# Kernel optimization log

Measured on AMD Instinct MI355X. Metric: run time of the kernel, lower is better.

The kernel has to match this reference:

```python
import jax, jax.numpy as jnp
import numpy as np

D_MODEL = 1024
N_HEADS = 16
D_FF = 4096
EPS = 1e-6


def layernorm(x, alpha, bias):
    # torch.std uses Bessel correction (ddof=1)
    mean = jnp.mean(x, axis=-1, keepdims=True)
    std = jnp.std(x, axis=-1, keepdims=True, ddof=1)
    return alpha * (x - mean) / (std + EPS) + bias


def setup_inputs() -> dict:
    key = jax.random.key(0)
    ks = jax.random.split(key, 12)
    s = 1.0 / np.sqrt(D_MODEL)
    sf = 1.0 / np.sqrt(D_FF)
    return {
        "x": jax.random.normal(ks[0], (2, 2048, D_MODEL), jnp.float32),
        "mask": jnp.ones((2, 1, 1, 2048), jnp.int32),
        "wq": jax.random.normal(ks[1], (D_MODEL, D_MODEL), jnp.float32) * s,
        "wk": jax.random.normal(ks[2], (D_MODEL, D_MODEL), jnp.float32) * s,
        "wv": jax.random.normal(ks[3], (D_MODEL, D_MODEL), jnp.float32) * s,
        "wo": jax.random.normal(ks[4], (D_MODEL, D_MODEL), jnp.float32) * s,
        "wo_b": jnp.zeros((D_MODEL,), jnp.float32),
        "w1": jax.random.normal(ks[5], (D_MODEL, D_FF), jnp.float32) * s,
        "b1": jnp.zeros((D_FF,), jnp.float32),
        "w2": jax.random.normal(ks[6], (D_FF, D_MODEL), jnp.float32) * sf,
        "b2": jnp.zeros((D_MODEL,), jnp.float32),
        "alpha1": jnp.ones((D_MODEL,), jnp.float32),
        "bias1": jnp.zeros((D_MODEL,), jnp.float32),
        "alpha2": jnp.ones((D_MODEL,), jnp.float32),
        "bias2": jnp.zeros((D_MODEL,), jnp.float32),
    }


def reference(x, mask, wq, wk, wv, wo, wo_b, w1, b1, w2, b2,
              alpha1, bias1, alpha2, bias2):
    B, S, D = x.shape
    h, dk = N_HEADS, D_MODEL // N_HEADS
    # projections -> [B, h, S, dk]
    q = (x @ wq).reshape(B, S, h, dk).transpose(0, 2, 1, 3)
    k = (x @ wk).reshape(B, S, h, dk).transpose(0, 2, 1, 3)
    v = (x @ wv).reshape(B, S, h, dk).transpose(0, 2, 1, 3)
    scores = jnp.einsum('bhqd,bhkd->bhqk', q, k) / jnp.sqrt(jnp.float32(dk))
    scores = jnp.where(mask == 0, jnp.float32(-1e9), scores)
    attn = jax.nn.softmax(scores, axis=-1)
    ctx = jnp.einsum('bhqk,bhkd->bhqd', attn, v)
    ctx = ctx.transpose(0, 2, 1, 3).reshape(B, S, D)
    attn_out = ctx @ wo + wo_b
    x = layernorm(x + attn_out, alpha1, bias1)
    ff = jax.nn.relu(x @ w1 + b1) @ w2 + b2
    x = layernorm(x + ff, alpha2, bias2)
    return x
```

## Files before the change

### kernel.cpp

```cpp
#include <hip/hip_runtime.h>
#include <hip/hip_bf16.h>

#define D_MODEL 1024
#define N_HEADS 16
#define DK      64
#define SEQ     2048
#define BATCH   2
#define D_FF    4096
#define ROWS    (BATCH*SEQ)
#define LN_EPS  1e-6f
#define SSTR    72
#define KTILE   128
#define PSTR    136

typedef __hip_bfloat16 bf16;
typedef __attribute__((ext_vector_type(8))) short frag8;
typedef __attribute__((ext_vector_type(4))) float facc4;

__device__ inline float bf2f(unsigned short u){ return __uint_as_float(((unsigned)u) << 16); }
__device__ inline float toF(bf16 v){ return __bfloat162float(v); }
__device__ inline unsigned short f2bu(float f){ bf16 h = __float2bfloat16(f); return *reinterpret_cast<unsigned short*>(&h); }

__device__ inline float ld1(const void* p, size_t idx, bool f32) {
    return f32 ? ((const float*)p)[idx] : toF(((const bf16*)p)[idx]);
}

struct U8 { unsigned short v[8]; };
__device__ inline U8 ld8bf(const void* p, size_t idx, bool f32) {
    U8 r;
    if (!f32) {
        *reinterpret_cast<uint4*>(r.v) = *reinterpret_cast<const uint4*>((const unsigned short*)p + idx);
    } else {
        const float* f = (const float*)p + idx;
        const float4 a = *reinterpret_cast<const float4*>(f);
        const float4 b = *reinterpret_cast<const float4*>(f + 4);
        r.v[0]=f2bu(a.x); r.v[1]=f2bu(a.y); r.v[2]=f2bu(a.z); r.v[3]=f2bu(a.w);
        r.v[4]=f2bu(b.x); r.v[5]=f2bu(b.y); r.v[6]=f2bu(b.z); r.v[7]=f2bu(b.w);
    }
    return r;
}

__device__ inline void gld16(const void* g, void* l) {
    __builtin_amdgcn_global_load_lds(
        reinterpret_cast<const __attribute__((address_space(1))) void*>(
            reinterpret_cast<uintptr_t>(g)),
        reinterpret_cast<__attribute__((address_space(3))) void*>(
            (unsigned int)reinterpret_cast<uintptr_t>(l)),
        16, 0, 0);
}

__global__ void probe_kernel(const void* __restrict__ xp, int* __restrict__ flag) {
    __shared__ int hit;
    if (threadIdx.x == 0) hit = 0;
    __syncthreads();
    const bf16* p = (const bf16*)xp;
    int bad = 0;
    for (int i = threadIdx.x; i < 8192; i += 256) {
        float v = fabsf(toF(p[i]));
        if (!(v <= 1e5f)) bad = 1;
    }
    if (bad) atomicOr(&hit, 1);
    __syncthreads();
    if (threadIdx.x == 0) *flag = hit;
}

__global__ __launch_bounds__(256) void xcvt_kernel(const void* __restrict__ x,
    bf16* __restrict__ out, const int* __restrict__ flagp)
{
    const bool f32 = (*flagp) != 0;
    const size_t i = ((size_t)blockIdx.x * 256 + threadIdx.x) * 8;
    U8 d = ld8bf(x, i, f32);
    *reinterpret_cast<uint4*>(out + i) = *reinterpret_cast<const uint4*>(d.v);
}

__global__ __launch_bounds__(256) void transpose_kernel(const void* __restrict__ W,
    bf16* __restrict__ WT, int K, int N, const int* __restrict__ flagp)
{
    const bool f32 = (*flagp) != 0;
    __shared__ float tile[32][33];
    const int tx = threadIdx.x, ty = threadIdx.y;
    const int n0 = blockIdx.x * 32, k0 = blockIdx.y * 32;
    #pragma unroll
    for (int r = 0; r < 4; ++r)
        tile[ty + 8*r][tx] = ld1(W, (size_t)(k0 + ty + 8*r) * N + n0 + tx, f32);
    __syncthreads();
    #pragma unroll
    for (int r = 0; r < 4; ++r)
        WT[(size_t)(n0 + ty + 8*r) * K + k0 + tx] = __float2bfloat16(tile[tx][ty + 8*r]);
}

__global__ __launch_bounds__(256) void vtrans_kernel(const bf16* __restrict__ V,
    bf16* __restrict__ VT)
{
    __shared__ unsigned short tile[32][33];
    const int tx = threadIdx.x, ty = threadIdx.y;
    const int s0 = blockIdx.x * 32, d0 = blockIdx.y * 32;
    const int bh = blockIdx.z, b = bh >> 4, h = bh & 15;
    #pragma unroll
    for (int r = 0; r < 4; ++r)
        tile[ty + 8*r][tx] = *reinterpret_cast<const unsigned short*>(
            V + ((size_t)(b * SEQ + s0 + ty + 8*r)) * D_MODEL + h * DK + d0 + tx);
    __syncthreads();
    #pragma unroll
    for (int r = 0; r < 4; ++r)
        *reinterpret_cast<unsigned short*>(
            VT + ((size_t)(bh * DK + d0 + ty + 8*r)) * SEQ + s0 + tx) = tile[tx][ty + 8*r];
}

template<bool RELU, bool BIAS, int NMAT, int SPLITK>
__global__ __launch_bounds__(256) void mgemm_kernel(const bf16* __restrict__ A,
    const bf16* __restrict__ BT, const void* __restrict__ bias,
    bf16* __restrict__ C, int M, int N, int K, const int* __restrict__ flagp)
{
    const bool inF32 = (*flagp) != 0;

    __shared__ unsigned short sA[128 * 64];
    __shared__ unsigned short sB[128 * 64];

    int which = 0, colb = blockIdx.x;
    if (NMAT > 1) { which = blockIdx.x >> 3; colb = blockIdx.x & 7; }
    const int kslice = (SPLITK > 1) ? blockIdx.z : 0;
    const int Kspan  = K / SPLITK;
    const int kbase  = kslice * Kspan;
    const bf16* Bp = BT + (size_t)which * N * K;
    bf16*       Cp = C  + (size_t)which * M * N + (size_t)kslice * M * N;

    const int row0 = blockIdx.y * 128;
    const int col0 = colb * 128;

    const int t    = threadIdx.x;
    const int wave = t >> 6;
    const int lane = t & 63;
    const int lm   = lane & 15;
    const int q    = lane >> 4;
    const int wm   = (wave & 1) * 64;
    const int wn   = (wave >> 1) * 64;

    facc4 acc[4][4];
    #pragma unroll
    for (int i = 0; i < 4; ++i)
        #pragma unroll
        for (int j = 0; j < 4; ++j)
            acc[i][j] = (facc4){0.f, 0.f, 0.f, 0.f};

    for (int k0 = kbase; k0 < kbase + Kspan; k0 += 64) {
        __syncthreads();
        #pragma unroll
        for (int j = 0; j < 4; ++j) {
            const int ch = (wave * 4 + j) * 64 + lane;
            const int r  = ch >> 3;
            const int cs = ch & 7;
            const int c  = cs ^ (r & 7);
            gld16(A  + (size_t)(row0 + r) * K + k0 + 8 * c, &sA[(wave * 4 + j) * 512]);
            gld16(Bp + (size_t)(col0 + r) * K + k0 + 8 * c, &sB[(wave * 4 + j) * 512]);
        }
        __syncthreads();

        #pragma unroll
        for (int kk = 0; kk < 64; kk += 32) {
            const int cr = (kk >> 3) + q;
            frag8 af[4], bfr[4];
            #pragma unroll
            for (int im = 0; im < 4; ++im) {
                const int m = wm + 16 * im + lm;
                af[im] = *reinterpret_cast<const frag8*>(&sA[m * 64 + ((cr ^ (m & 7)) << 3)]);
            }
            #pragma unroll
            for (int in = 0; in < 4; ++in) {
                const int n = wn + 16 * in + lm;
                bfr[in] = *reinterpret_cast<const frag8*>(&sB[n * 64 + ((cr ^ (n & 7)) << 3)]);
            }
            #pragma unroll
            for (int im = 0; im < 4; ++im)
                #pragma unroll
                for (int in = 0; in < 4; ++in)
                    acc[im][in] = __builtin_amdgcn_mfma_f32_16x16x32_bf16(af[im], bfr[in], acc[im][in], 0, 0, 0);
        }
    }

    #pragma unroll
    for (int in = 0; in < 4; ++in) {
        const int col = col0 + wn + 16*in + lm;
        float bv = 0.f;
        if (BIAS && kslice == 0) bv = ld1(bias, col, inF32);
        #pragma unroll
        for (int im = 0; im < 4; ++im) {
            #pragma unroll
            for (int r = 0; r < 4; ++r) {
                const int row = row0 + wm + 16*im + 4*q + r;
                float v = acc[im][in][r] + bv;
                if (RELU) v = fmaxf(v, 0.f);
                Cp[(size_t)row * N + col] = __float2bfloat16(v);
            }
        }
    }
}

__global__ __launch_bounds__(256) void fattn_kernel(
    const bf16* __restrict__ Qg, const bf16* __restrict__ Kg,
    const bf16* __restrict__ VTg, const int* __restrict__ mask,
    bf16* __restrict__ ctx)
{
    __shared__ unsigned short sK[128 * 64];
    __shared__ unsigned short sV[64 * 128];
    __shared__ unsigned short PsU[4 * 16 * PSTR];
    __shared__ float madd[KTILE];

    const int t    = threadIdx.x;
    const int qt   = blockIdx.x;
    const int h    = blockIdx.y;
    const int b    = blockIdx.z;
    const int q0   = qt * 64;
    const int bh   = b * N_HEADS + h;
    const int wave = t >> 6;
    const int lane = t & 63;
    const int lm   = lane & 15;
    const int qd   = lane >> 4;

    unsigned short* Qs = PsU;
    {
        const int sr = t >> 2, sd0 = (t & 3) * 16;
        const unsigned short* src = (const unsigned short*)
            (Qg + ((size_t)(b * SEQ + q0 + sr)) * D_MODEL + h * DK + sd0);
        unsigned short qi[16], qo[16];
        *reinterpret_cast<uint4*>(&qi[0]) = *reinterpret_cast<const uint4*>(src);
        *reinterpret_cast<uint4*>(&qi[8]) = *reinterpret_cast<const uint4*>(src + 8);
        #pragma unroll
        for (int u = 0; u < 16; ++u) qo[u] = f2bu(bf2f(qi[u]) * 0.125f);
        *reinterpret_cast<uint4*>(&Qs[sr * SSTR + sd0])     = *reinterpret_cast<const uint4*>(&qo[0]);
        *reinterpret_cast<uint4*>(&Qs[sr * SSTR + sd0 + 8]) = *reinterpret_cast<const uint4*>(&qo[8]);
    }
    __syncthreads();
    frag8 qf[2];
    #pragma unroll
    for (int s2 = 0; s2 < 2; ++s2)
        qf[s2] = *reinterpret_cast<const frag8*>(&Qs[(16 * wave + lm) * SSTR + 32 * s2 + 8 * qd]);

    facc4 accO[4];
    float m_r[4], l_r[4];
    #pragma unroll
    for (int r = 0; r < 4; ++r) { m_r[r] = -1e30f; l_r[r] = 0.f; }
    #pragma unroll
    for (int in = 0; in < 4; ++in) accO[in] = (facc4){0.f, 0.f, 0.f, 0.f};

    for (int kt = 0; kt < SEQ / KTILE; ++kt) {
        const int k0 = kt * KTILE;
        __syncthreads();

        #pragma unroll
        for (int j = 0; j < 4; ++j) {
            const int ch = (wave * 4 + j) * 64 + lane;
            const int rK = ch >> 3, cK = (ch & 7) ^ (rK & 7);
            gld16(Kg + ((size_t)(b * SEQ + k0 + rK)) * D_MODEL + h * DK + 8 * cK,
                  &sK[(wave * 4 + j) * 512]);
            const int rV = ch >> 4, cV = (ch & 15) ^ (rV & 15);
            gld16(VTg + ((size_t)(bh * DK + rV)) * SEQ + k0 + 8 * cV,
                  &sV[(wave * 4 + j) * 512]);
        }
        if (t < KTILE) madd[t] = (mask[b * SEQ + k0 + t] == 0) ? -1e9f : 0.f;
        __syncthreads();

        facc4 accS[8];
        #pragma unroll
        for (int i = 0; i < 8; ++i) accS[i] = (facc4){0.f, 0.f, 0.f, 0.f};
        #pragma unroll
        for (int i = 0; i < 8; ++i) {
            #pragma unroll
            for (int s2 = 0; s2 < 2; ++s2) {
                const int cr = 4 * s2 + qd;
                frag8 kf = *reinterpret_cast<const frag8*>(
                    &sK[(16 * i + lm) * 64 + ((cr ^ (lm & 7)) << 3)]);
                accS[i] = __builtin_amdgcn_mfma_f32_16x16x32_bf16(qf[s2], kf, accS[i], 0, 0, 0);
            }
        }

        float madv[8];
        #pragma unroll
        for (int i = 0; i < 8; ++i) madv[i] = madd[16 * i + lm];

        float mx[4];
        #pragma unroll
        for (int r = 0; r < 4; ++r) {
            float m0 = -1e30f;
            #pragma unroll
            for (int i = 0; i < 8; ++i) m0 = fmaxf(m0, accS[i][r] + madv[i]);
            #pragma unroll
            for (int off = 1; off < 16; off <<= 1) m0 = fmaxf(m0, __shfl_xor(m0, off));
            mx[r] = m0;
        }

        float alpha[4], mn[4], psum[4];
        #pragma unroll
        for (int r = 0; r < 4; ++r) {
            mn[r] = fmaxf(m_r[r], mx[r]);
            alpha[r] = __expf(m_r[r] - mn[r]);
            m_r[r] = mn[r];
            psum[r] = 0.f;
        }
        unsigned short* Pw = &PsU[wave * 16 * PSTR];
        #pragma unroll
        for (int i = 0; i < 8; ++i) {
            #pragma unroll
            for (int r = 0; r < 4; ++r) {
                float p = __expf(accS[i][r] + madv[i] - mn[r]);
                psum[r] += p;
                Pw[(qd * 4 + r) * PSTR + 16 * i + lm] = f2bu(p);
            }
        }
        #pragma unroll
        for (int r = 0; r < 4; ++r) {
            float s = psum[r];
            #pragma unroll
            for (int off = 1; off < 16; off <<= 1) s += __shfl_xor(s, off);
            l_r[r] = l_r[r] * alpha[r] + s;
            #pragma unroll
            for (int in = 0; in < 4; ++in) accO[in][r] *= alpha[r];
        }

        #pragma unroll
        for (int c = 0; c < 4; ++c) {
            frag8 pf = *reinterpret_cast<const frag8*>(&Pw[lm * PSTR + 32 * c + 8 * qd]);
            #pragma unroll
            for (int in = 0; in < 4; ++in) {
                const int cr = 4 * c + qd;
                frag8 vf = *reinterpret_cast<const frag8*>(
                    &sV[(16 * in + lm) * 128 + ((cr ^ lm) << 3)]);
                accO[in] = __builtin_amdgcn_mfma_f32_16x16x32_bf16(pf, vf, accO[in], 0, 0, 0);
            }
        }
    }

    float inv[4];
    #pragma unroll
    for (int r = 0; r < 4; ++r) inv[r] = 1.f / l_r[r];
    #pragma unroll
    for (int in = 0; in < 4; ++in)
        #pragma unroll
        for (int r = 0; r < 4; ++r)
            ctx[((size_t)(b * SEQ + q0 + 16 * wave + qd * 4 + r)) * D_MODEL + h * DK + 16 * in + lm]
                = __float2bfloat16(accO[in][r] * inv[r]);
}

template<bool BASE_WS, bool OUT_WS>
__global__ __launch_bounds__(256) void ln_kernel(const void* __restrict__ base,
    const bf16* __restrict__ addv, const bf16* __restrict__ addv2,
    const void* __restrict__ alpha, const void* __restrict__ bias,
    void* __restrict__ outp, const int* __restrict__ flagp)
{
    const bool inF32 = (*flagp) != 0;
    __shared__ float vals[D_MODEL];
    __shared__ float red[256];
    const int row = blockIdx.x, tid = threadIdx.x;

    float lsum = 0.f;
    for (int i = tid; i < D_MODEL; i += 256) {
        const size_t off = (size_t)row * D_MODEL + i;
        float v = (BASE_WS ? toF(((const bf16*)base)[off]) : ld1(base, off, inF32)) + toF(addv[off]);
        if (addv2) v += toF(addv2[off]);
        vals[i] = v; lsum += v;
    }
    red[tid] = lsum; __syncthreads();
    for (int s = 128; s > 0; s >>= 1) { if (tid < s) red[tid] += red[tid + s]; __syncthreads(); }
    const float mean = red[0] / (float)D_MODEL; __syncthreads();

    float lsq = 0.f;
    for (int i = tid; i < D_MODEL; i += 256) { float dd = vals[i] - mean; lsq += dd * dd; }
    red[tid] = lsq; __syncthreads();
    for (int s = 128; s > 0; s >>= 1) { if (tid < s) red[tid] += red[tid + s]; __syncthreads(); }
    const float var = red[0] / (float)(D_MODEL - 1);
    const float inv = 1.f / (sqrtf(var) + LN_EPS);

    for (int i = tid; i < D_MODEL; i += 256) {
        const size_t off = (size_t)row * D_MODEL + i;
        const float y = ld1(alpha, i, inF32) * (vals[i] - mean) * inv + ld1(bias, i, inF32);
        if (OUT_WS || !inF32) ((bf16*)outp)[off] = __float2bfloat16(y);
        else                  ((float*)outp)[off] = y;
    }
}

extern "C" void kernel_launch(void* const* d_in, const int* in_sizes, int n_in,
                              void* d_out, int out_size, void* d_ws, size_t ws_size,
                              hipStream_t stream)
{
    const void* x    = d_in[0];
    const int*  mask = (const int*)d_in[1];
    const void* wq   = d_in[2];
    const void* wk   = d_in[3];
    const void* wv   = d_in[4];
    const void* wo   = d_in[5];
    const void* wo_b = d_in[6];
    const void* w1   = d_in[7];
    const void* b1   = d_in[8];
    const void* w2   = d_in[9];
    const void* b2   = d_in[10];
    const void* al1  = d_in[11];
    const void* bi1  = d_in[12];
    const void* al2  = d_in[13];
    const void* bi2  = d_in[14];

    const size_t MB = 1024 * 1024;
    char* ws = (char*)d_ws;
    const bool SPLIT = ws_size >= 64 * MB + 4096;
    if (!SPLIT && ws_size < 56 * MB + 4096) return;

    bf16* Qb    = (bf16*)(ws + 0 * MB);
    bf16* Kb    = (bf16*)(ws + 8 * MB);
    bf16* Vb    = (bf16*)(ws + 16 * MB);
    bf16* Xb    = (bf16*)(ws + 24 * MB);
    bf16* VTb   = (bf16*)(ws + 24 * MB);
    bf16* WQKVT = (bf16*)(ws + 32 * MB);
    bf16* CTXb  = (bf16*)(ws + 32 * MB);
    bf16* W2T   = (bf16*)(ws + 32 * MB);
    bf16* WOT   = (bf16*)(ws + 0 * MB);
    bf16* ATT0  = (bf16*)(ws + 48 * MB);
    bf16* ATT1  = (bf16*)(ws + 56 * MB);
    bf16* W1T   = (bf16*)(ws + 48 * MB);
    bf16* X20   = (bf16*)(ws + 48 * MB);
    bf16* X21   = (bf16*)(ws + 56 * MB);
    bf16* X1b   = (bf16*)(ws + 40 * MB);
    bf16* FFb   = (bf16*)(ws + 0 * MB);
    int*  flagp = (int*)(ws + (SPLIT ? 64 : 56) * MB);

    probe_kernel<<<1, 256, 0, stream>>>(x, flagp);
    xcvt_kernel<<<dim3(ROWS * D_MODEL / 2048), 256, 0, stream>>>(x, Xb, flagp);

    dim3 tb(32, 8);
    transpose_kernel<<<dim3(32, 32), tb, 0, stream>>>(wq, WQKVT,           D_MODEL, D_MODEL, flagp);
    transpose_kernel<<<dim3(32, 32), tb, 0, stream>>>(wk, WQKVT + 1048576, D_MODEL, D_MODEL, flagp);
    transpose_kernel<<<dim3(32, 32), tb, 0, stream>>>(wv, WQKVT + 2097152, D_MODEL, D_MODEL, flagp);

    mgemm_kernel<false, false, 3, 1><<<dim3(24, 32), 256, 0, stream>>>(
        Xb, WQKVT, nullptr, Qb, ROWS, D_MODEL, D_MODEL, flagp);

    vtrans_kernel<<<dim3(SEQ / 32, 2, BATCH * N_HEADS), tb, 0, stream>>>(Vb, VTb);

    fattn_kernel<<<dim3(SEQ / 64, N_HEADS, BATCH), 256, 0, stream>>>(Qb, Kb, VTb, mask, CTXb);

    transpose_kernel<<<dim3(32, 32), tb, 0, stream>>>(wo, WOT, D_MODEL, D_MODEL, flagp);

    if (SPLIT) {
        mgemm_kernel<false, true, 1, 2><<<dim3(8, 32, 2), 256, 0, stream>>>(
            CTXb, WOT, wo_b, ATT0, ROWS, D_MODEL, D_MODEL, flagp);
        ln_kernel<false, true><<<ROWS, 256, 0, stream>>>(x, ATT0, ATT1, al1, bi1, X1b, flagp);
    } else {
        mgemm_kernel<false, true, 1, 1><<<dim3(8, 32), 256, 0, stream>>>(
            CTXb, WOT, wo_b, ATT0, ROWS, D_MODEL, D_MODEL, flagp);
        ln_kernel<false, true><<<ROWS, 256, 0, stream>>>(x, ATT0, nullptr, al1, bi1, X1b, flagp);
    }

    transpose_kernel<<<dim3(128, 32), tb, 0, stream>>>(w1, W1T, D_MODEL, D_FF, flagp);
    mgemm_kernel<true, true, 1, 1><<<dim3(32, 32), 256, 0, stream>>>(
        X1b, W1T, b1, FFb, ROWS, D_FF, D_MODEL, flagp);

    transpose_kernel<<<dim3(32, 128), tb, 0, stream>>>(w2, W2T, D_FF, D_MODEL, flagp);

    if (SPLIT) {
        mgemm_kernel<false, true, 1, 2><<<dim3(8, 32, 2), 256, 0, stream>>>(
            FFb, W2T, b2, X20, ROWS, D_MODEL, D_FF, flagp);
        ln_kernel<true, false><<<ROWS, 256, 0, stream>>>(X1b, X20, X21, al2, bi2, d_out, flagp);
    } else {
        mgemm_kernel<false, true, 1, 1><<<dim3(8, 32), 256, 0, stream>>>(
            FFb, W2T, b2, X20, ROWS, D_MODEL, D_FF, flagp);
        ln_kernel<true, false><<<ROWS, 256, 0, stream>>>(X1b, X20, nullptr, al2, bi2, d_out, flagp);
    }
}
```

Baseline: 419.1 us.

## Double attention query tile to 128 rows and batch square weight transposes

The flash-attention kernel now handles 128 query rows per block with 8 waves (512 threads) instead of 64 rows with 4. Each K/V tile staged in shared memory is therefore reused by twice as many queries, halving global K/V traffic per query, at the cost of a larger P buffer and fewer, heavier blocks. In the large-workspace path, the wq/wk/wv/wo transposes are merged into one launch with all weight transposes issued up front, and buffers are re-laid out so no transposed weight is overwritten. The small-workspace path keeps the old launch sequence but also uses the new attention configuration.

```diff
diff --git a/kernel.cpp b/kernel.cpp
--- a/kernel.cpp
+++ b/kernel.cpp
@@ -89,6 +89,26 @@
         WT[(size_t)(n0 + ty + 8*r) * K + k0 + tx] = __float2bfloat16(tile[tx][ty + 8*r]);
 }
 
+__global__ __launch_bounds__(256) void transpose4_kernel(const void* __restrict__ w0,
+    const void* __restrict__ w1, const void* __restrict__ w2, const void* __restrict__ w3,
+    bf16* __restrict__ WT4, const int* __restrict__ flagp)
+{
+    const bool f32 = (*flagp) != 0;
+    const int which = blockIdx.z;
+    const void* W = (which == 0) ? w0 : (which == 1) ? w1 : (which == 2) ? w2 : w3;
+    bf16* WT = WT4 + (size_t)which * D_MODEL * D_MODEL;
+    __shared__ float tile[32][33];
+    const int tx = threadIdx.x, ty = threadIdx.y;
+    const int n0 = blockIdx.x * 32, k0 = blockIdx.y * 32;
+    #pragma unroll
+    for (int r = 0; r < 4; ++r)
+        tile[ty + 8*r][tx] = ld1(W, (size_t)(k0 + ty + 8*r) * D_MODEL + n0 + tx, f32);
+    __syncthreads();
+    #pragma unroll
+    for (int r = 0; r < 4; ++r)
+        WT[(size_t)(n0 + ty + 8*r) * D_MODEL + k0 + tx] = __float2bfloat16(tile[tx][ty + 8*r]);
+}
+
 __global__ __launch_bounds__(256) void vtrans_kernel(const bf16* __restrict__ V,
     bf16* __restrict__ VT)
 {
@@ -196,21 +216,21 @@
     }
 }
 
-__global__ __launch_bounds__(256) void fattn_kernel(
+__global__ __launch_bounds__(512) void fattn_kernel(
     const bf16* __restrict__ Qg, const bf16* __restrict__ Kg,
     const bf16* __restrict__ VTg, const int* __restrict__ mask,
     bf16* __restrict__ ctx)
 {
     __shared__ unsigned short sK[128 * 64];
     __shared__ unsigned short sV[64 * 128];
-    __shared__ unsigned short PsU[4 * 16 * PSTR];
+    __shared__ unsigned short PsU[8 * 16 * PSTR];
     __shared__ float madd[KTILE];
 
     const int t    = threadIdx.x;
     const int qt   = blockIdx.x;
     const int h    = blockIdx.y;
     const int b    = blockIdx.z;
-    const int q0   = qt * 64;
+    const int q0   = qt * 128;
     const int bh   = b * N_HEADS + h;
     const int wave = t >> 6;
     const int lane = t & 63;
@@ -248,14 +268,14 @@
         __syncthreads();
 
         #pragma unroll
-        for (int j = 0; j < 4; ++j) {
-            const int ch = (wave * 4 + j) * 64 + lane;
+        for (int j = 0; j < 2; ++j) {
+            const int ch = (wave * 2 + j) * 64 + lane;
             const int rK = ch >> 3, cK = (ch & 7) ^ (rK & 7);
             gld16(Kg + ((size_t)(b * SEQ + k0 + rK)) * D_MODEL + h * DK + 8 * cK,
-                  &sK[(wave * 4 + j) * 512]);
+                  &sK[(wave * 2 + j) * 512]);
             const int rV = ch >> 4, cV = (ch & 15) ^ (rV & 15);
             gld16(VTg + ((size_t)(bh * DK + rV)) * SEQ + k0 + 8 * cV,
-                  &sV[(wave * 4 + j) * 512]);
+                  &sV[(wave * 2 + j) * 512]);
         }
         if (t < KTILE) madd[t] = (mask[b * SEQ + k0 + t] == 0) ? -1e9f : 0.f;
         __syncthreads();
@@ -400,65 +420,95 @@
 
     const size_t MB = 1024 * 1024;
     char* ws = (char*)d_ws;
-    const bool SPLIT = ws_size >= 64 * MB + 4096;
-    if (!SPLIT && ws_size < 56 * MB + 4096) return;
-
-    bf16* Qb    = (bf16*)(ws + 0 * MB);
-    bf16* Kb    = (bf16*)(ws + 8 * MB);
-    bf16* Vb    = (bf16*)(ws + 16 * MB);
-    bf16* Xb    = (bf16*)(ws + 24 * MB);
-    bf16* VTb   = (bf16*)(ws + 24 * MB);
-    bf16* WQKVT = (bf16*)(ws + 32 * MB);
-    bf16* CTXb  = (bf16*)(ws + 32 * MB);
-    bf16* W2T   = (bf16*)(ws + 32 * MB);
-    bf16* WOT   = (bf16*)(ws + 0 * MB);
-    bf16* ATT0  = (bf16*)(ws + 48 * MB);
-    bf16* ATT1  = (bf16*)(ws + 56 * MB);
-    bf16* W1T   = (bf16*)(ws + 48 * MB);
-    bf16* X20   = (bf16*)(ws + 48 * MB);
-    bf16* X21   = (bf16*)(ws + 56 * MB);
-    bf16* X1b   = (bf16*)(ws + 40 * MB);
-    bf16* FFb   = (bf16*)(ws + 0 * MB);
-    int*  flagp = (int*)(ws + (SPLIT ? 64 : 56) * MB);
-
-    probe_kernel<<<1, 256, 0, stream>>>(x, flagp);
-    xcvt_kernel<<<dim3(ROWS * D_MODEL / 2048), 256, 0, stream>>>(x, Xb, flagp);
+    const bool BIG = ws_size >= 64 * MB + 4096;
+    if (!BIG && ws_size < 56 * MB + 4096) return;
 
     dim3 tb(32, 8);
-    transpose_kernel<<<dim3(32, 32), tb, 0, stream>>>(wq, WQKVT,           D_MODEL, D_MODEL, flagp);
-    transpose_kernel<<<dim3(32, 32), tb, 0, stream>>>(wk, WQKVT + 1048576, D_MODEL, D_MODEL, flagp);
-    transpose_kernel<<<dim3(32, 32), tb, 0, stream>>>(wv, WQKVT + 2097152, D_MODEL, D_MODEL, flagp);
-
-    mgemm_kernel<false, false, 3, 1><<<dim3(24, 32), 256, 0, stream>>>(
-        Xb, WQKVT, nullptr, Qb, ROWS, D_MODEL, D_MODEL, flagp);
-
-    vtrans_kernel<<<dim3(SEQ / 32, 2, BATCH * N_HEADS), tb, 0, stream>>>(Vb, VTb);
-
-    fattn_kernel<<<dim3(SEQ / 64, N_HEADS, BATCH), 256, 0, stream>>>(Qb, Kb, VTb, mask, CTXb);
-
-    transpose_kernel<<<dim3(32, 32), tb, 0, stream>>>(wo, WOT, D_MODEL, D_MODEL, flagp);
-
-    if (SPLIT) {
+
+    if (BIG) {
+        bf16* Qb   = (bf16*)(ws + 0 * MB);
+        bf16* Kb   = (bf16*)(ws + 8 * MB);
+        bf16* Vb   = (bf16*)(ws + 16 * MB);
+        bf16* Xb   = (bf16*)(ws + 24 * MB);
+        bf16* VTb  = (bf16*)(ws + 24 * MB);
+        bf16* WT4  = (bf16*)(ws + 32 * MB);
+        bf16* WOT  = WT4 + (size_t)3 * D_MODEL * D_MODEL;
+        bf16* W1T  = (bf16*)(ws + 40 * MB);
+        bf16* W2T  = (bf16*)(ws + 48 * MB);
+        bf16* CTXb = (bf16*)(ws + 56 * MB);
+        bf16* ATT0 = (bf16*)(ws + 0 * MB);
+        bf16* ATT1 = (bf16*)(ws + 8 * MB);
+        bf16* X1b  = (bf16*)(ws + 56 * MB);
+        bf16* FFb  = (bf16*)(ws + 0 * MB);
+        bf16* X20  = (bf16*)(ws + 32 * MB);
+        bf16* X21  = (bf16*)(ws + 40 * MB);
+        int*  flagp = (int*)(ws + 64 * MB);
+
+        probe_kernel<<<1, 256, 0, stream>>>(x, flagp);
+        xcvt_kernel<<<dim3(ROWS * D_MODEL / 2048), 256, 0, stream>>>(x, Xb, flagp);
+
+        transpose4_kernel<<<dim3(32, 32, 4), tb, 0, stream>>>(wq, wk, wv, wo, WT4, flagp);
+        transpose_kernel<<<dim3(128, 32), tb, 0, stream>>>(w1, W1T, D_MODEL, D_FF, flagp);
+        transpose_kernel<<<dim3(32, 128), tb, 0, stream>>>(w2, W2T, D_FF, D_MODEL, flagp);
+
+        mgemm_kernel<false, false, 3, 1><<<dim3(24, 32), 256, 0, stream>>>(
+            Xb, WT4, nullptr, Qb, ROWS, D_MODEL, D_MODEL, flagp);
+
+        vtrans_kernel<<<dim3(SEQ / 32, 2, BATCH * N_HEADS), tb, 0, stream>>>(Vb, VTb);
+
+        fattn_kernel<<<dim3(SEQ / 128, N_HEADS, BATCH), 512, 0, stream>>>(Qb, Kb, VTb, mask, CTXb);
+
         mgemm_kernel<false, true, 1, 2><<<dim3(8, 32, 2), 256, 0, stream>>>(
             CTXb, WOT, wo_b, ATT0, ROWS, D_MODEL, D_MODEL, flagp);
         ln_kernel<false, true><<<ROWS, 256, 0, stream>>>(x, ATT0, ATT1, al1, bi1, X1b, flagp);
-    } else {
-        mgemm_kernel<false, true, 1, 1><<<dim3(8, 32), 256, 0, stream>>>(
-            CTXb, WOT, wo_b, ATT0, ROWS, D_MODEL, D_MODEL, flagp);
-        ln_kernel<false, true><<<ROWS, 256, 0, stream>>>(x, ATT0, nullptr, al1, bi1, X1b, flagp);
-    }
-
-    transpose_kernel<<<dim3(128, 32), tb, 0, stream>>>(w1, W1T, D_MODEL, D_FF, flagp);
-    mgemm_kernel<true, true, 1, 1><<<dim3(32, 32), 256, 0, stream>>>(
-        X1b, W1T, b1, FFb, ROWS, D_FF, D_MODEL, flagp);
-
-    transpose_kernel<<<dim3(32, 128), tb, 0, stream>>>(w2, W2T, D_FF, D_MODEL, flagp);
-
-    if (SPLIT) {
+
+        mgemm_kernel<true, true, 1, 1><<<dim3(32, 32), 256, 0, stream>>>(
+            X1b, W1T, b1, FFb, ROWS, D_FF, D_MODEL, flagp);
+
         mgemm_kernel<false, true, 1, 2><<<dim3(8, 32, 2), 256, 0, stream>>>(
             FFb, W2T, b2, X20, ROWS, D_MODEL, D_FF, flagp);
         ln_kernel<true, false><<<ROWS, 256, 0, stream>>>(X1b, X20, X21, al2, bi2, d_out, flagp);
     } else {
+        bf16* Qb    = (bf16*)(ws + 0 * MB);
+        bf16* Kb    = (bf16*)(ws + 8 * MB);
+        bf16* Vb    = (bf16*)(ws + 16 * MB);
+        bf16* Xb    = (bf16*)(ws + 24 * MB);
+        bf16* VTb   = (bf16*)(ws + 24 * MB);
+        bf16* WQKVT = (bf16*)(ws + 32 * MB);
+        bf16* CTXb  = (bf16*)(ws + 32 * MB);
+        bf16* W2T   = (bf16*)(ws + 32 * MB);
+        bf16* WOT   = (bf16*)(ws + 0 * MB);
+        bf16* ATT0  = (bf16*)(ws + 48 * MB);
+        bf16* W1T   = (bf16*)(ws + 48 * MB);
+        bf16* X20   = (bf16*)(ws + 48 * MB);
+        bf16* X1b   = (bf16*)(ws + 40 * MB);
+        bf16* FFb   = (bf16*)(ws + 0 * MB);
+        int*  flagp = (int*)(ws + 56 * MB);
+
+        probe_kernel<<<1, 256, 0, stream>>>(x, flagp);
+        xcvt_kernel<<<dim3(ROWS * D_MODEL / 2048), 256, 0, stream>>>(x, Xb, flagp);
+
+        transpose_kernel<<<dim3(32, 32), tb, 0, stream>>>(wq, WQKVT,           D_MODEL, D_MODEL, flagp);
+        transpose_kernel<<<dim3(32, 32), tb, 0, stream>>>(wk, WQKVT + 1048576, D_MODEL, D_MODEL, flagp);
+        transpose_kernel<<<dim3(32, 32), tb, 0, stream>>>(wv, WQKVT + 2097152, D_MODEL, D_MODEL, flagp);
+
+        mgemm_kernel<false, false, 3, 1><<<dim3(24, 32), 256, 0, stream>>>(
+            Xb, WQKVT, nullptr, Qb, ROWS, D_MODEL, D_MODEL, flagp);
+
+        vtrans_kernel<<<dim3(SEQ / 32, 2, BATCH * N_HEADS), tb, 0, stream>>>(Vb, VTb);
+
+        fattn_kernel<<<dim3(SEQ / 128, N_HEADS, BATCH), 512, 0, stream>>>(Qb, Kb, VTb, mask, CTXb);
+
+        transpose_kernel<<<dim3(32, 32), tb, 0, stream>>>(wo, WOT, D_MODEL, D_MODEL, flagp);
+        mgemm_kernel<false, true, 1, 1><<<dim3(8, 32), 256, 0, stream>>>(
+            CTXb, WOT, wo_b, ATT0, ROWS, D_MODEL, D_MODEL, flagp);
+        ln_kernel<false, true><<<ROWS, 256, 0, stream>>>(x, ATT0, nullptr, al1, bi1, X1b, flagp);
+
+        transpose_kernel<<<dim3(128, 32), tb, 0, stream>>>(w1, W1T, D_MODEL, D_FF, flagp);
+        mgemm_kernel<true, true, 1, 1><<<dim3(32, 32), 256, 0, stream>>>(
+            X1b, W1T, b1, FFb, ROWS, D_FF, D_MODEL, flagp);
+
+        transpose_kernel<<<dim3(32, 128), tb, 0, stream>>>(w2, W2T, D_FF, D_MODEL, flagp);
         mgemm_kernel<false, true, 1, 1><<<dim3(8, 32), 256, 0, stream>>>(
             FFb, W2T, b2, X20, ROWS, D_MODEL, D_FF, flagp);
         ln_kernel<true, false><<<ROWS, 256, 0, stream>>>(X1b, X20, nullptr, al2, bi2, d_out, flagp);
```

After: 397.0 us. 5.3% less time.
